# Optimization experiments

Hardware: AMD Instinct MI355X
Metric: run time of the kernel (lower is better)

## Reference

```python
import jax, jax.numpy as jnp
import numpy as np

B, T, L, D, H = 4, 8, 197, 512, 8
DK = D // H
SIM_TH = 0.0
N = T * (L - 1)  # 1568 local tokens

def _ln(x, g, b, eps=1e-5):
    x32 = x.astype(jnp.float32)
    m = jnp.mean(x32, axis=-1, keepdims=True)
    v = jnp.mean((x32 - m) ** 2, axis=-1, keepdims=True)
    return (((x32 - m) * jax.lax.rsqrt(v + eps)) * g + b).astype(x.dtype)

def _qgelu(x):
    return x * jax.nn.sigmoid(1.702 * x)

def _mha(x, w_in, b_in, w_out, b_out):
    # torch nn.MultiheadAttention, x: [S, Bt, D] (seq-first)
    S, Bt, _ = x.shape
    qkv = x @ w_in.T + b_in
    q, k, v = jnp.split(qkv, 3, axis=-1)
    q = q.reshape(S, Bt, H, DK); k = k.reshape(S, Bt, H, DK); v = v.reshape(S, Bt, H, DK)
    scores = jnp.einsum('sbhd,tbhd->bhst', q, k) / jnp.sqrt(jnp.asarray(DK, x.dtype))
    p = jax.nn.softmax(scores, axis=-1)
    o = jnp.einsum('bhst,tbhd->sbhd', p, v).reshape(S, Bt, D)
    return o @ w_out.T + b_out

def _resblock(x, ln1g, ln1b, inw, inb, outw, outb, ln2g, ln2b, fcw, fcb, pw, pb):
    x = x + _mha(_ln(x, ln1g, ln1b), inw, inb, outw, outb)
    h = _qgelu(_ln(x, ln2g, ln2b) @ fcw.T + fcb)
    return x + h @ pw.T + pb

def _build_graph(x, g_mask):
    xd = jax.lax.stop_gradient(x)  # matches x.detach()
    xn = xd / jnp.maximum(jnp.linalg.norm(xd, axis=-1, keepdims=True), 1e-12)
    sim = jnp.einsum('bnd,bmd->bnm', xn, xn)
    adj = jnp.where(sim < SIM_TH, 0.0, sim)
    return adj * g_mask  # t != 1 branch

def _graph_attn(x, mask, wq, bq, wk, bk, wv, bv, wo, bo):
    Bb, Nn, _ = x.shape
    def heads(a):
        return a.reshape(Bb, Nn, H, DK).transpose(0, 2, 1, 3)
    Q = heads(x @ wq.T + bq); K = heads(x @ wk.T + bk); V = heads(x @ wv.T + bv)
    scores = jnp.einsum('bhnd,bhmd->bhnm', Q, K) / jnp.sqrt(jnp.asarray(DK, x.dtype))
    m = mask[:, None]  # [b,1,N,N]
    scores = jnp.where(m == 0, -jnp.inf, scores * m)  # scores*mask then masked_fill(mask==0,-inf)
    p = jax.nn.softmax(scores, axis=-1)
    o = jnp.einsum('bhnm,bhmd->bhnd', p, V).transpose(0, 2, 1, 3).reshape(Bb, Nn, D)
    return o @ wo.T + bo

def _forward(x, proj_w, proj_b,
             m_ln1g, m_ln1b, m_inw, m_inb, m_outw, m_outb,
             m_ln2g, m_ln2b, m_fcw, m_fcb, m_pw, m_pb,
             g_wq, g_bq, g_wk, g_bk, g_wv, g_bv, g_wo, g_bo,
             ln1g, ln1b, a_inw, a_inb, a_outw, a_outb,
             ln2g, ln2b, fcw, fcb, pw, pb, g_mask):
    b, t, l, d = x.shape
    x = x @ proj_w.T + proj_b
    glob = x[:, :, 0, :].transpose(1, 0, 2)  # [t,b,d]
    msg = (m_ln1g, m_ln1b, m_inw, m_inb, m_outw, m_outb, m_ln2g, m_ln2b, m_fcw, m_fcb, m_pw, m_pb)
    glob = _resblock(glob, *msg)
    glob = _resblock(glob, *msg)  # message_attn applied twice (shared weights)
    glob = glob.reshape(1, t, b, d)
    loc = x[:, :, 1:, :].reshape(b, t * (l - 1), d)
    gm = _build_graph(loc, g_mask)
    loc = _graph_attn(loc, gm, g_wq, g_bq, g_wk, g_bk, g_wv, g_bv, g_wo, g_bo)
    loc = loc.reshape(b, t, l - 1, d).transpose(2, 1, 0, 3)  # [l-1,t,b,d]
    y = jnp.concatenate([glob, loc], axis=0).reshape(l, t * b, d)
    y = y + _mha(_ln(y, ln1g, ln1b), a_inw, a_inb, a_outw, a_outb)
    y = y + _qgelu(_ln(y, ln2g, ln2b) @ fcw.T + fcb) @ pw.T + pb
    return y.reshape(l, t, b, d).transpose(2, 1, 0, 3)  # [b,t,l,d]

def setup_inputs() -> dict:
    key = jax.random.key(0)
    ks = jax.random.split(key, 64)
    s = 0.02
    def w(i, shape):
        return jax.random.normal(ks[i], shape, jnp.float32) * s
    ones = jnp.ones((D,), jnp.float32); zeros = jnp.zeros((D,), jnp.float32)
    gm = (jax.random.uniform(ks[60], (N, N)) < 0.5).astype(jnp.float32)
    gm = gm.at[jnp.arange(N), jnp.arange(N)].set(1.0)  # keep self-edges so no row is fully masked
    return dict(
        x=jax.random.normal(ks[0], (B, T, L, D), jnp.float32),
        proj_w=w(1, (D, D)), proj_b=jnp.zeros((D,), jnp.float32),
        m_ln1g=ones, m_ln1b=zeros,
        m_inw=w(2, (3 * D, D)), m_inb=jnp.zeros((3 * D,), jnp.float32),
        m_outw=w(3, (D, D)), m_outb=zeros,
        m_ln2g=ones, m_ln2b=zeros,
        m_fcw=w(4, (4 * D, D)), m_fcb=jnp.zeros((4 * D,), jnp.float32),
        m_pw=w(5, (D, 4 * D)), m_pb=zeros,
        g_wq=w(6, (D, D)), g_bq=zeros, g_wk=w(7, (D, D)), g_bk=zeros,
        g_wv=w(8, (D, D)), g_bv=zeros, g_wo=w(9, (D, D)), g_bo=zeros,
        ln1g=ones, ln1b=zeros,
        a_inw=w(10, (3 * D, D)), a_inb=jnp.zeros((3 * D,), jnp.float32),
        a_outw=w(11, (D, D)), a_outb=zeros,
        ln2g=ones, ln2b=zeros,
        fcw=w(12, (4 * D, D)), fcb=jnp.zeros((4 * D,), jnp.float32),
        pw=w(13, (D, 4 * D)), pb=zeros,
        g_mask=gm,
    )

def reference(x, proj_w, proj_b, m_ln1g, m_ln1b, m_inw, m_inb, m_outw, m_outb,
              m_ln2g, m_ln2b, m_fcw, m_fcb, m_pw, m_pb,
              g_wq, g_bq, g_wk, g_bk, g_wv, g_bv, g_wo, g_bo,
              ln1g, ln1b, a_inw, a_inb, a_outw, a_outb,
              ln2g, ln2b, fcw, fcb, pw, pb, g_mask):
    return _forward(x, proj_w, proj_b, m_ln1g, m_ln1b, m_inw, m_inb, m_outw, m_outb,
                    m_ln2g, m_ln2b, m_fcw, m_fcb, m_pw, m_pb,
                    g_wq, g_bq, g_wk, g_bk, g_wv, g_bv, g_wo, g_bo,
                    ln1g, ln1b, a_inw, a_inb, a_outw, a_outb,
                    ln2g, ln2b, fcw, fcb, pw, pb, g_mask)
```

## Files before the change

### kernel.cpp

```cpp
#include <hip/hip_runtime.h>
#include <hip/hip_bf16.h>

typedef unsigned short u16;
typedef __attribute__((ext_vector_type(8))) short bf16x8;
typedef __attribute__((ext_vector_type(4))) float f32x4;

#define FINF __builtin_huge_valf()

static __device__ __forceinline__ float bf2f(u16 v){ union{unsigned u; float f;} c; c.u = ((unsigned)v)<<16; return c.f; }
static __device__ __forceinline__ u16 f2bf(float f){ union{__hip_bfloat16 h; u16 u;} c; c.h = __float2bfloat16(f); return c.u; }
static __device__ __forceinline__ bf16x8 scale8(bf16x8 v, float s){
  bf16x8 o;
  #pragma unroll
  for (int e=0;e<8;e++) o[e] = (short)f2bf(bf2f((u16)v[e])*s);
  return o;
}

static __device__ __forceinline__ void gload16(const void* g, void* l){
  __builtin_amdgcn_global_load_lds(
      (const __attribute__((address_space(1))) void*)g,
      (__attribute__((address_space(3))) void*)l, 16, 0, 0);
}

#define WAIT_VM0()   { asm volatile("s_waitcnt vmcnt(0)" ::: "memory"); __builtin_amdgcn_sched_barrier(0); }
#define BARRIER()    { __builtin_amdgcn_sched_barrier(0); __builtin_amdgcn_s_barrier(); __builtin_amdgcn_sched_barrier(0); }

struct CvtArgs {
  const float* src[14];
  u16* dst[14];
  int n[14];
};
__global__ __launch_bounds__(256) void cvt_multi(CvtArgs a){
  int seg = blockIdx.y;
  const float* s = a.src[seg]; u16* d = a.dst[seg]; int n = a.n[seg];
  for (int i = (blockIdx.x*256 + threadIdx.x)*4; i < n; i += gridDim.x*256*4){
    float4 v = *(const float4*)(s + i);
    ushort4 o = { f2bf(v.x), f2bf(v.y), f2bf(v.z), f2bf(v.w) };
    *(ushort4*)(d + i) = o;
  }
}

__global__ __launch_bounds__(256) void concat_bias(const float* a, const float* b, const float* c, float* o){
  int i = blockIdx.x*256 + threadIdx.x;
  o[i] = i < 512 ? a[i] : (i < 1024 ? b[i-512] : c[i-1024]);
}

template<int BM, int EPI, int MW>
__global__ __launch_bounds__(256,MW) void gemm_nt(
    const u16* __restrict__ A, const u16* __restrict__ Bw,
    const float* __restrict__ bias, const float* aux, void* out,
    int M, int Nn, int K, int ldc, long aBatch, long bBatch, long cBatch)
{
  constexpr int MI = BM/32;
  constexpr int WSPAN = BM/2;
  __shared__ __align__(16) u16 a_lds[2*BM*64];
  __shared__ __align__(16) u16 b_lds[2*128*64];
  const int z = blockIdx.z;
  const u16* Az = A + (long)z*aBatch;
  const u16* Bz = Bw + (long)z*bBatch;
  const int n0 = blockIdx.x*128, m0 = blockIdx.y*BM;
  const int t = threadIdx.x, lane = t & 63, wave = t >> 6;
  const int wr = wave >> 1, wc = wave & 1;
  const int r = lane & 15, kq = lane >> 4;

  const int srow = t >> 3;
  const int scol = ((t&7)*8) ^ ((srow&7)<<3);
  int rowA[MI], rowB[4];
  #pragma unroll
  for (int i=0;i<MI;i++){ int ga = m0 + i*32 + srow; rowA[i] = ga < M ? ga : M-1; }
  #pragma unroll
  for (int i=0;i<4;i++){ int gb = n0 + i*32 + srow; rowB[i] = gb < Nn ? gb : Nn-1; }

  f32x4 acc[MI][4] = {};
  const int nkt = K >> 6;

  auto STAGE = [&](int kt, int buf){
    const long koff = (long)kt*64 + scol;
    #pragma unroll
    for (int i=0;i<MI;i++)
      gload16(Az + (long)rowA[i]*K + koff, (char*)a_lds + buf*(BM*128) + i*4096 + wave*1024);
    #pragma unroll
    for (int i=0;i<4;i++)
      gload16(Bz + (long)rowB[i]*K + koff, (char*)b_lds + buf*16384 + i*4096 + wave*1024);
  };

  STAGE(0,0);
  WAIT_VM0(); BARRIER();
  for (int kt=0; kt<nkt; kt++){
    const int cur = kt&1;
    if (kt+1 < nkt) STAGE(kt+1, cur^1);
    const u16* al = a_lds + cur*BM*64;
    const u16* bl = b_lds + cur*8192;
    #pragma unroll
    for (int kk=0; kk<2; kk++){
      bf16x8 af[MI], bfr[4];
      #pragma unroll
      for (int i=0;i<MI;i++){
        int rw = wr*WSPAN + i*16 + r;
        af[i] = *(const bf16x8*)&al[rw*64 + ((kk*32 + kq*8) ^ ((rw&7)<<3))];
      }
      #pragma unroll
      for (int j=0;j<4;j++){
        int rw = wc*64 + j*16 + r;
        bfr[j] = *(const bf16x8*)&bl[rw*64 + ((kk*32 + kq*8) ^ ((rw&7)<<3))];
      }
      #pragma unroll
      for (int i=0;i<MI;i++)
        #pragma unroll
        for (int j=0;j<4;j++)
          acc[i][j] = __builtin_amdgcn_mfma_f32_16x16x32_bf16(af[i], bfr[j], acc[i][j], 0,0,0);
    }
    WAIT_VM0(); BARRIER();
  }

  #pragma unroll
  for (int i=0;i<MI;i++){
    #pragma unroll
    for (int j=0;j<4;j++){
      int gcol = n0 + wc*64 + j*16 + r;
      if (gcol >= Nn) continue;
      float bv = bias ? bias[gcol] : 0.f;
      #pragma unroll
      for (int rr=0; rr<4; rr++){
        int grow = m0 + wr*WSPAN + i*16 + kq*4 + rr;
        if (grow >= M) continue;
        float v = acc[i][j][rr] + bv;
        if constexpr (EPI==0){
          ((float*)out)[(long)z*cBatch + (long)grow*ldc + gcol] = v;
        } else if constexpr (EPI==1){
          ((u16*)out)[(long)z*cBatch + (long)grow*ldc + gcol] = f2bf(v);
        } else if constexpr (EPI==2){
          long idx = (long)z*cBatch + (long)grow*ldc + gcol;
          ((float*)out)[idx] = aux[idx] + v;
        } else if constexpr (EPI==3){
          float g = v / (1.f + __expf(-1.702f*v));
          ((u16*)out)[(long)z*cBatch + (long)grow*ldc + gcol] = f2bf(g);
        } else if constexpr (EPI==4){
          float adj = v < 0.f ? 0.f : v;
          float gmv = aux[(long)grow*Nn + gcol];
          ((u16*)out)[(long)z*cBatch + (long)grow*ldc + gcol] = f2bf(adj*gmv);
        } else if constexpr (EPI==5){
          int b = grow/1568, n = grow%1568, tt = n/196, lp = n%196;
          int yrow = (1+lp)*32 + tt*4 + b;
          ((float*)out)[(long)yrow*ldc + gcol] = v;
        } else if constexpr (EPI==6){
          long idx = (long)grow*ldc + gcol;
          int l = grow>>5, rb = grow&31, tt = rb>>2, bb = rb&3;
          ((float*)out)[((long)((bb*8+tt)*197) + l)*512 + gcol] = aux[idx] + v;
        }
      }
    }
  }
}

__global__ __launch_bounds__(256) void transpose_v(
    const u16* __restrict__ src, u16* __restrict__ vt,
    int nrows, long zofs, long nofs, int vcol0, int outld)
{
  __shared__ u16 tile[64][66];
  const int t = threadIdx.x;
  const int nt = blockIdx.x, h = blockIdx.y, z = blockIdx.z;
  const int n0 = nt*64;
  const int rlo = t>>3, c0 = (t&7)*8;
  #pragma unroll
  for (int i=0;i<2;i++){
    int nl = i*32 + rlo;
    int n = n0 + nl; int nc = n < nrows ? n : nrows-1;
    const u16* s = src + (long)z*zofs + (long)nc*nofs + vcol0 + h*64 + c0;
    uint4 v = *(const uint4*)s;
    bool dead = n >= nrows;
    #pragma unroll
    for (int e=0;e<8;e++) tile[nl][c0+e] = dead ? (u16)0 : ((const u16*)&v)[e];
  }
  __syncthreads();
  #pragma unroll
  for (int i=0;i<2;i++){
    int d = i*32 + rlo;
    u16 tmp[8];
    #pragma unroll
    for (int e=0;e<8;e++) tmp[e] = tile[c0+e][d];
    int ncol = n0 + c0;
    if (ncol + 8 <= outld){
      u16* dst = vt + ((long)((z*8+h)*64 + d))*outld + ncol;
      *(uint4*)dst = *(uint4*)tmp;
    }
  }
}

template<bool MASKED>
__global__ __launch_bounds__(256, MASKED?2:3) void flash2(
    const u16* __restrict__ QKV, const u16* __restrict__ VT,
    const u16* __restrict__ gmask, u16* __restrict__ Out,
    int nq, int nk, int nqb, long qBatch, long qRow,
    long oBatch, long oRow, long gmBatch, int vtld)
{
  __shared__ __align__(16) u16 k_lds[2*4096];
  __shared__ __align__(16) u16 v_lds[2*4096];
  __shared__ __align__(16) u16 g_lds[MASKED ? 2*4096 : 8];
  __shared__ __align__(16) u16 p_lds[4][16*72];
  int h, z, qb;
  if constexpr (MASKED){
    int id = blockIdx.x;
    int a = id>>6, c = id&7; h = (id>>3)&7;
    int G = a*8 + c;
    if (G >= 4*nqb) return;
    z = G / nqb; qb = G % nqb;
  } else {
    qb = blockIdx.x; h = blockIdx.y; z = blockIdx.z;
  }
  const int t = threadIdx.x, lane = t&63, wave = t>>6;
  const int r = lane&15, kq = lane>>4;
  const u16* Qb = QKV + (long)z*qBatch + h*64;
  const u16* Kb = Qb + 512;
  const u16* Vt = VT + (long)(z*8+h)*64*vtld;
  const u16* Gz = MASKED ? (gmask + (long)z*gmBatch) : nullptr;
  const int qt0 = qb*64;
  const int q0  = qt0 + wave*16;

  bf16x8 qf0, qf1;
  { int qi = q0 + r; if (qi > nq-1) qi = nq-1;
    const u16* qp = Qb + (long)qi*qRow + kq*8;
    qf0 = scale8(*(const bf16x8*)qp, 0.125f);
    qf1 = scale8(*(const bf16x8*)(qp+32), 0.125f); }

  const int srow = t>>3;
  const int scol = ((t&7)*8) ^ ((srow&7)<<3);

  auto stage = [&](int kt, int buf){
    #pragma unroll
    for (int i=0;i<2;i++){
      int j = kt*64 + i*32 + srow; if (j > nk-1) j = nk-1;
      gload16(Kb + (long)j*qRow + scol, (char*)k_lds + buf*8192 + i*4096 + wave*1024);
    }
    #pragma unroll
    for (int i=0;i<2;i++){
      int d = i*32 + srow;
      gload16(Vt + (long)d*vtld + kt*64 + scol, (char*)v_lds + buf*8192 + i*4096 + wave*1024);
    }
    if constexpr (MASKED){
      #pragma unroll
      for (int i=0;i<2;i++){
        int qr = qt0 + i*32 + srow; if (qr > nq-1) qr = nq-1;
        gload16(Gz + (long)qr*nk + kt*64 + scol, (char*)g_lds + buf*8192 + i*4096 + wave*1024);
      }
    }
  };

  bf16x8 ONES;
  #pragma unroll
  for (int e=0;e<8;e++) ONES[e] = (short)0x3F80;

  float m_[4] = {-FINF,-FINF,-FINF,-FINF};
  f32x4 o_[4] = {}; f32x4 ol = {};

  const int nkt = (nk + 63) >> 6;
  stage(0,0);
  __syncthreads();
  for (int kt=0; kt<nkt; kt++){
    const int cur = kt&1;
    if (kt+1 < nkt) stage(kt+1, cur^1);

    float s[4][4];
    const u16* kl = k_lds + cur*4096;
    #pragma unroll
    for (int sub=0; sub<4; sub++){
      int rw = sub*16 + r; int sw = (rw&7)<<3;
      bf16x8 kf0 = *(const bf16x8*)&kl[rw*64 + ((kq*8) ^ sw)];
      bf16x8 kf1 = *(const bf16x8*)&kl[rw*64 + ((32 + kq*8) ^ sw)];
      f32x4 sc = {};
      sc = __builtin_amdgcn_mfma_f32_16x16x32_bf16(qf0, kf0, sc, 0,0,0);
      sc = __builtin_amdgcn_mfma_f32_16x16x32_bf16(qf1, kf1, sc, 0,0,0);
      #pragma unroll
      for (int rr=0;rr<4;rr++) s[sub][rr] = sc[rr];
    }
    #pragma unroll
    for (int sub=0; sub<4; sub++){
      int key = kt*64 + sub*16 + r;
      bool kdead = key >= nk;
      #pragma unroll
      for (int rr=0;rr<4;rr++){
        float sv = s[sub][rr];
        if constexpr (MASKED){
          int lrow = wave*16 + kq*4 + rr;
          u16 g = g_lds[cur*4096 + lrow*64 + ((sub*16+r) ^ ((lrow&7)<<3))];
          if (g == 0 || kdead) sv = -FINF; else sv *= bf2f(g);
        } else {
          if (kdead) sv = -FINF;
        }
        s[sub][rr] = sv;
      }
    }
    #pragma unroll
    for (int rr=0;rr<4;rr++){
      float mx = fmaxf(fmaxf(s[0][rr],s[1][rr]), fmaxf(s[2][rr],s[3][rr]));
      #pragma unroll
      for (int d=1; d<16; d<<=1) mx = fmaxf(mx, __shfl_xor(mx, d));
      float mnew = fmaxf(m_[rr], mx);
      float fac = (m_[rr] == -FINF) ? 0.f : __expf(m_[rr] - mnew);
      #pragma unroll
      for (int sub=0;sub<4;sub++)
        s[sub][rr] = (s[sub][rr] == -FINF) ? 0.f : __expf(s[sub][rr] - mnew);
      m_[rr] = mnew;
      o_[0][rr]*=fac; o_[1][rr]*=fac; o_[2][rr]*=fac; o_[3][rr]*=fac; ol[rr]*=fac;
    }
    #pragma unroll
    for (int rr=0;rr<4;rr++){
      int prow = kq*4+rr;
      #pragma unroll
      for (int sub=0;sub<4;sub++)
        p_lds[wave][prow*72 + ((sub*16+r) ^ ((prow&7)<<3))] = f2bf(s[sub][rr]);
    }
    const u16* vl = v_lds + cur*4096;
    #pragma unroll
    for (int c=0;c<2;c++){
      bf16x8 pf = *(const bf16x8*)&p_lds[wave][r*72 + ((c*32 + kq*8) ^ ((r&7)<<3))];
      #pragma unroll
      for (int j=0;j<4;j++){
        int rw = j*16 + r;
        bf16x8 vf = *(const bf16x8*)&vl[rw*64 + ((c*32 + kq*8) ^ ((rw&7)<<3))];
        o_[j] = __builtin_amdgcn_mfma_f32_16x16x32_bf16(pf, vf, o_[j], 0,0,0);
      }
      ol = __builtin_amdgcn_mfma_f32_16x16x32_bf16(pf, ONES, ol, 0,0,0);
    }
    __syncthreads();
  }

  #pragma unroll
  for (int rr=0;rr<4;rr++){
    int qrow = q0 + kq*4 + rr;
    if (qrow >= nq) continue;
    float inv = ol[rr] > 0.f ? 1.f/ol[rr] : 0.f;
    #pragma unroll
    for (int j=0;j<4;j++)
      Out[(long)z*oBatch + (long)qrow*oRow + h*64 + j*16 + r] = f2bf(o_[j][rr]*inv);
  }
}

__global__ __launch_bounds__(256) void ln_rows(const float* __restrict__ in,
    const float* __restrict__ g, const float* __restrict__ b, u16* __restrict__ out, int rows)
{
  int wave = threadIdx.x >> 6, lane = threadIdx.x & 63;
  int row = blockIdx.x*4 + wave;
  if (row >= rows) return;
  const float4* x = (const float4*)(in + (long)row*512);
  float4 v0 = x[lane], v1 = x[lane+64];
  float s  = v0.x+v0.y+v0.z+v0.w + v1.x+v1.y+v1.z+v1.w;
  float ss = v0.x*v0.x+v0.y*v0.y+v0.z*v0.z+v0.w*v0.w + v1.x*v1.x+v1.y*v1.y+v1.z*v1.z+v1.w*v1.w;
  #pragma unroll
  for (int d=1; d<64; d<<=1){ s += __shfl_xor(s,d); ss += __shfl_xor(ss,d); }
  float mean = s * (1.f/512.f);
  float var = ss * (1.f/512.f) - mean*mean;
  float rs = rsqrtf(var + 1e-5f);
  const float4* gg = (const float4*)g; const float4* bb = (const float4*)b;
  float4 g0 = gg[lane], g1 = gg[lane+64], b0 = bb[lane], b1 = bb[lane+64];
  u16* o = out + (long)row*512;
  ushort4 o0 = { f2bf((v0.x-mean)*rs*g0.x + b0.x), f2bf((v0.y-mean)*rs*g0.y + b0.y),
                 f2bf((v0.z-mean)*rs*g0.z + b0.z), f2bf((v0.w-mean)*rs*g0.w + b0.w) };
  ushort4 o1 = { f2bf((v1.x-mean)*rs*g1.x + b1.x), f2bf((v1.y-mean)*rs*g1.y + b1.y),
                 f2bf((v1.z-mean)*rs*g1.z + b1.z), f2bf((v1.w-mean)*rs*g1.w + b1.w) };
  *(ushort4*)(o + lane*4) = o0;
  *(ushort4*)(o + 256 + lane*4) = o1;
}

__global__ __launch_bounds__(256) void locprep(const float* __restrict__ y0,
    u16* __restrict__ xn, u16* __restrict__ locb)
{
  int wave = threadIdx.x >> 6, lane = threadIdx.x & 63;
  int rr = blockIdx.x*4 + wave;
  int bb = rr/1568, n = rr%1568, tt = n/196, lp = n%196;
  const float4* x = (const float4*)(y0 + ((long)((bb*8+tt)*197) + 1 + lp)*512);
  float4 v0 = x[lane], v1 = x[lane+64];
  float ss = v0.x*v0.x+v0.y*v0.y+v0.z*v0.z+v0.w*v0.w + v1.x*v1.x+v1.y*v1.y+v1.z*v1.z+v1.w*v1.w;
  #pragma unroll
  for (int d=1; d<64; d<<=1) ss += __shfl_xor(ss,d);
  float sc = 1.f / fmaxf(sqrtf(ss), 1e-12f);
  u16* ox = xn + (long)rr*512;
  u16* ol = locb + (long)rr*512;
  ushort4 a0 = { f2bf(v0.x*sc), f2bf(v0.y*sc), f2bf(v0.z*sc), f2bf(v0.w*sc) };
  ushort4 a1 = { f2bf(v1.x*sc), f2bf(v1.y*sc), f2bf(v1.z*sc), f2bf(v1.w*sc) };
  ushort4 c0 = { f2bf(v0.x), f2bf(v0.y), f2bf(v0.z), f2bf(v0.w) };
  ushort4 c1 = { f2bf(v1.x), f2bf(v1.y), f2bf(v1.z), f2bf(v1.w) };
  *(ushort4*)(ox + lane*4) = a0;  *(ushort4*)(ox + 256 + lane*4) = a1;
  *(ushort4*)(ol + lane*4) = c0;  *(ushort4*)(ol + 256 + lane*4) = c1;
}

__global__ __launch_bounds__(64) void msg_attn(const u16* __restrict__ mqkv, u16* __restrict__ matt){
  __shared__ float q_s[8][64], k_s[8][64], v_s[8][64];
  int bh = blockIdx.x; int bt = bh>>3, h = bh&7;
  int lane = threadIdx.x;
  int row = lane>>3, cc = (lane&7)*8;
  #pragma unroll
  for (int e=0;e<8;e++){
    long base = (long)(row*4 + bt)*1536 + h*64 + cc + e;
    q_s[row][cc+e] = bf2f(mqkv[base]);
    k_s[row][cc+e] = bf2f(mqkv[base + 512]);
    v_s[row][cc+e] = bf2f(mqkv[base + 1024]);
  }
  __syncthreads();
  int q = lane>>3, k = lane&7;
  float s = 0.f;
  #pragma unroll 16
  for (int d=0; d<64; d++) s += q_s[q][d]*k_s[k][d];
  s *= 0.125f;
  float mx = s;
  #pragma unroll
  for (int d=1; d<8; d<<=1) mx = fmaxf(mx, __shfl_xor(mx,d));
  float p = __expf(s - mx), ps = p;
  #pragma unroll
  for (int d=1; d<8; d<<=1) ps += __shfl_xor(ps,d);
  p /= ps;
  for (int d=0; d<64; d++){
    float ov = p * v_s[k][d];
    #pragma unroll
    for (int m=1; m<8; m<<=1) ov += __shfl_xor(ov,m);
    if (k == (d>>3)) matt[(long)(q*4 + bt)*512 + h*64 + d] = f2bf(ov);
  }
}

__global__ __launch_bounds__(256) void gather_glob(const float* __restrict__ y0, float* __restrict__ glob){
  int idx = blockIdx.x*256 + threadIdx.x;
  int orow = idx>>9, d = idx&511;
  int tt = orow>>2, bb = orow&3;
  glob[idx] = y0[((long)(bb*8+tt)*197)*512 + d];
}
__global__ __launch_bounds__(256) void copy32(const float* __restrict__ glob, float* __restrict__ y){
  int idx = blockIdx.x*256 + threadIdx.x;
  y[idx] = glob[idx];
}

extern "C" void kernel_launch(void* const* d_in, const int* in_sizes, int n_in,
                              void* d_out, int out_size, void* d_ws, size_t ws_size,
                              hipStream_t stream)
{
  const float* x      = (const float*)d_in[0];
  const float* proj_w = (const float*)d_in[1];
  const float* proj_b = (const float*)d_in[2];
  const float* m_ln1g = (const float*)d_in[3];
  const float* m_ln1b = (const float*)d_in[4];
  const float* m_inw  = (const float*)d_in[5];
  const float* m_inb  = (const float*)d_in[6];
  const float* m_outw = (const float*)d_in[7];
  const float* m_outb = (const float*)d_in[8];
  const float* m_ln2g = (const float*)d_in[9];
  const float* m_ln2b = (const float*)d_in[10];
  const float* m_fcw  = (const float*)d_in[11];
  const float* m_fcb  = (const float*)d_in[12];
  const float* m_pw   = (const float*)d_in[13];
  const float* m_pb   = (const float*)d_in[14];
  const float* g_wq = (const float*)d_in[15]; const float* g_bq = (const float*)d_in[16];
  const float* g_wk = (const float*)d_in[17]; const float* g_bk = (const float*)d_in[18];
  const float* g_wv = (const float*)d_in[19]; const float* g_bv = (const float*)d_in[20];
  const float* g_wo = (const float*)d_in[21]; const float* g_bo = (const float*)d_in[22];
  const float* ln1g = (const float*)d_in[23]; const float* ln1b = (const float*)d_in[24];
  const float* a_inw = (const float*)d_in[25]; const float* a_inb = (const float*)d_in[26];
  const float* a_outw = (const float*)d_in[27]; const float* a_outb = (const float*)d_in[28];
  const float* ln2g = (const float*)d_in[29]; const float* ln2b = (const float*)d_in[30];
  const float* fcw = (const float*)d_in[31]; const float* fcb = (const float*)d_in[32];
  const float* pw = (const float*)d_in[33]; const float* pb = (const float*)d_in[34];
  const float* g_mask = (const float*)d_in[35];

  if (ws_size < (size_t)99753984) return;

  char* ws = (char*)d_ws;
  u16* WB = (u16*)ws;
  const long WPROJ=0, WMIN=262144, WMOUT=1048576, WMFC=1310720, WMP=2359296,
             WGQ=3407872, WGK=3670016, WGV=3932160, WGO=4194304,
             WAIN=4456448, WAOUT=5242880, WFC=5505024, WP=6553600;
  float* y0   = (float*)(ws + 15204352);
  float* y    = (float*)(ws + 28114944);
  u16* lnbuf  = (u16*)(ws + 41025536);
  u16* vtg    = (u16*)(ws + 41025536);
  u16* locb   = (u16*)(ws + 47480832);
  u16* qkv    = (u16*)(ws + 53903360);
  u16* xb     = (u16*)(ws + 73269248);
  u16* gm     = (u16*)(ws + 73269248);
  u16* vt2    = (u16*)(ws + 73269248);
  u16* hbuf   = (u16*)(ws + 73269248);
  u16* obuf   = (u16*)(ws + 92938240);
  float* glob = (float*)(ws + 99393536);
  u16* mlnb   = (u16*)(ws + 99459072);
  u16* mqkv   = (u16*)(ws + 99491840);
  u16* matt   = (u16*)(ws + 99590144);
  u16* mh     = (u16*)(ws + 99622912);
  float* gbias = (float*)(ws + 99622912);

  CvtArgs ca;
  auto setseg=[&](int i, const float* s, u16* d, int n){ ca.src[i]=s; ca.dst[i]=d; ca.n[i]=n; };
  setseg(0,  x,      xb,       6304*512);
  setseg(1,  proj_w, WB+WPROJ, 262144);
  setseg(2,  m_inw,  WB+WMIN,  786432);
  setseg(3,  m_outw, WB+WMOUT, 262144);
  setseg(4,  m_fcw,  WB+WMFC,  1048576);
  setseg(5,  m_pw,   WB+WMP,   1048576);
  setseg(6,  g_wq,   WB+WGQ,   262144);
  setseg(7,  g_wk,   WB+WGK,   262144);
  setseg(8,  g_wv,   WB+WGV,   262144);
  setseg(9,  g_wo,   WB+WGO,   262144);
  setseg(10, a_inw,  WB+WAIN,  786432);
  setseg(11, a_outw, WB+WAOUT, 262144);
  setseg(12, fcw,    WB+WFC,   1048576);
  setseg(13, pw,     WB+WP,    1048576);
  cvt_multi<<<dim3(128,14), 256, 0, stream>>>(ca);

  gemm_nt<64,0,3><<<dim3(4,99), 256, 0, stream>>>(xb, WB+WPROJ, proj_b, nullptr, y0, 6304,512,512,512, 0,0,0);

  gather_glob<<<64,256,0,stream>>>(y0, glob);

  for (int it=0; it<2; ++it){
    ln_rows<<<8,256,0,stream>>>(glob, m_ln1g, m_ln1b, mlnb, 32);
    gemm_nt<64,1,3><<<dim3(12,1),256,0,stream>>>(mlnb, WB+WMIN, m_inb, nullptr, mqkv, 32,1536,512,1536, 0,0,0);
    msg_attn<<<32,64,0,stream>>>(mqkv, matt);
    gemm_nt<64,2,3><<<dim3(4,1),256,0,stream>>>(matt, WB+WMOUT, m_outb, glob, glob, 32,512,512,512, 0,0,0);
    ln_rows<<<8,256,0,stream>>>(glob, m_ln2g, m_ln2b, mlnb, 32);
    gemm_nt<64,3,3><<<dim3(16,1),256,0,stream>>>(mlnb, WB+WMFC, m_fcb, nullptr, mh, 32,2048,512,2048, 0,0,0);
    gemm_nt<64,2,3><<<dim3(4,1),256,0,stream>>>(mh, WB+WMP, m_pb, glob, glob, 32,512,2048,512, 0,0,0);
  }

  concat_bias<<<6,256,0,stream>>>(g_bq, g_bk, g_bv, gbias);

  locprep<<<1568,256,0,stream>>>(y0, lnbuf, locb);

  gemm_nt<128,4,2><<<dim3(13,13,4),256,0,stream>>>(lnbuf, lnbuf, nullptr, g_mask, gm,
      1568,1568,512,1568, 1568L*512, 1568L*512, 1568L*1568);

  gemm_nt<128,1,2><<<dim3(12,49),256,0,stream>>>(locb, WB+WGQ, gbias, nullptr, qkv, 6272,1536,512,1536, 0,0,0);

  transpose_v<<<dim3(25,8,4),256,0,stream>>>(qkv, vtg, 1568, 1568L*1536, 1536L, 1024, 1568);

  flash2<true><<<832,256,0,stream>>>(qkv, vtg, gm, obuf,
      1568,1568,25, 1568L*1536, 1536, 1568L*512, 512, 1568L*1568, 1568);

  gemm_nt<64,5,3><<<dim3(4,98),256,0,stream>>>(obuf, WB+WGO, g_bo, nullptr, y, 6272,512,512,512, 0,0,0);

  copy32<<<64,256,0,stream>>>(glob, y);

  ln_rows<<<1576,256,0,stream>>>(y, ln1g, ln1b, lnbuf, 6304);
  gemm_nt<128,1,2><<<dim3(12,50),256,0,stream>>>(lnbuf, WB+WAIN, a_inb, nullptr, qkv, 6304,1536,512,1536, 0,0,0);
  transpose_v<<<dim3(4,8,32),256,0,stream>>>(qkv, vt2, 197, 1536L, 32L*1536, 1024, 256);
  flash2<false><<<dim3(4,8,32),256,0,stream>>>(qkv, vt2, nullptr, obuf,
      197,197,4, 1536, 32L*1536, 512, 32L*512, 0, 256);
  gemm_nt<64,2,3><<<dim3(4,99),256,0,stream>>>(obuf, WB+WAOUT, a_outb, y, y, 6304,512,512,512, 0,0,0);

  ln_rows<<<1576,256,0,stream>>>(y, ln2g, ln2b, lnbuf, 6304);
  gemm_nt<128,3,2><<<dim3(16,50),256,0,stream>>>(lnbuf, WB+WFC, fcb, nullptr, hbuf, 6304,2048,512,2048, 0,0,0);
  gemm_nt<64,6,3><<<dim3(4,99),256,0,stream>>>(hbuf, WB+WP, pb, y, (float*)d_out, 6304,512,2048,512, 0,0,0);
}
```

Before: 608.0 us.

## Transpose flash attention to key-major scores, load V and mask directly into registers

The attention kernel now computes S^T by swapping the MFMA operands. Each lane then holds one query row, so the row max needs only two cross-lane shuffles instead of a 16-lane butterfly. V fragments and graph-mask values are loaded from global memory straight into registers instead of being staged through LDS, which cuts LDS to the K double buffer plus a P tile and raises the occupancy target to 4 blocks. Several large GEMMs also switch from 128-row tiles to 64-row tiles with more blocks, trading data reuse for higher occupancy. The unstaged global loads of V and the mask may add latency, since they are no longer overlapped by the async LDS pipeline.

```diff
diff --git a/kernel.cpp b/kernel.cpp
--- a/kernel.cpp
+++ b/kernel.cpp
@@ -188,16 +188,14 @@
 }
 
 template<bool MASKED>
-__global__ __launch_bounds__(256, MASKED?2:3) void flash2(
+__global__ __launch_bounds__(256,4) void flash3(
     const u16* __restrict__ QKV, const u16* __restrict__ VT,
     const u16* __restrict__ gmask, u16* __restrict__ Out,
     int nq, int nk, int nqb, long qBatch, long qRow,
     long oBatch, long oRow, long gmBatch, int vtld)
 {
   __shared__ __align__(16) u16 k_lds[2*4096];
-  __shared__ __align__(16) u16 v_lds[2*4096];
-  __shared__ __align__(16) u16 g_lds[MASKED ? 2*4096 : 8];
-  __shared__ __align__(16) u16 p_lds[4][16*72];
+  __shared__ __align__(16) u16 p_lds[4][1024];
   int h, z, qb;
   if constexpr (MASKED){
     int id = blockIdx.x;
@@ -213,126 +211,129 @@
   const u16* Qb = QKV + (long)z*qBatch + h*64;
   const u16* Kb = Qb + 512;
   const u16* Vt = VT + (long)(z*8+h)*64*vtld;
-  const u16* Gz = MASKED ? (gmask + (long)z*gmBatch) : nullptr;
   const int qt0 = qb*64;
   const int q0  = qt0 + wave*16;
+  const int q   = q0 + r;
+  const int qc  = q < nq ? q : nq-1;
+  const u16* Gq = MASKED ? (gmask + (long)z*gmBatch + (long)qc*nk) : nullptr;
 
   bf16x8 qf0, qf1;
-  { int qi = q0 + r; if (qi > nq-1) qi = nq-1;
-    const u16* qp = Qb + (long)qi*qRow + kq*8;
+  { const u16* qp = Qb + (long)qc*qRow + kq*8;
     qf0 = scale8(*(const bf16x8*)qp, 0.125f);
     qf1 = scale8(*(const bf16x8*)(qp+32), 0.125f); }
 
   const int srow = t>>3;
   const int scol = ((t&7)*8) ^ ((srow&7)<<3);
 
-  auto stage = [&](int kt, int buf){
+  auto stage_k = [&](int kt, int buf){
     #pragma unroll
     for (int i=0;i<2;i++){
       int j = kt*64 + i*32 + srow; if (j > nk-1) j = nk-1;
       gload16(Kb + (long)j*qRow + scol, (char*)k_lds + buf*8192 + i*4096 + wave*1024);
     }
-    #pragma unroll
-    for (int i=0;i<2;i++){
-      int d = i*32 + srow;
-      gload16(Vt + (long)d*vtld + kt*64 + scol, (char*)v_lds + buf*8192 + i*4096 + wave*1024);
-    }
-    if constexpr (MASKED){
-      #pragma unroll
-      for (int i=0;i<2;i++){
-        int qr = qt0 + i*32 + srow; if (qr > nq-1) qr = nq-1;
-        gload16(Gz + (long)qr*nk + kt*64 + scol, (char*)g_lds + buf*8192 + i*4096 + wave*1024);
-      }
-    }
   };
 
   bf16x8 ONES;
   #pragma unroll
   for (int e=0;e<8;e++) ONES[e] = (short)0x3F80;
 
-  float m_[4] = {-FINF,-FINF,-FINF,-FINF};
-  f32x4 o_[4] = {}; f32x4 ol = {};
+  float m_ = -FINF;
+  f32x4 o_[4] = {};  f32x4 l_ = {};
 
   const int nkt = (nk + 63) >> 6;
-  stage(0,0);
+  stage_k(0,0);
   __syncthreads();
   for (int kt=0; kt<nkt; kt++){
     const int cur = kt&1;
-    if (kt+1 < nkt) stage(kt+1, cur^1);
-
-    float s[4][4];
+    if (kt+1 < nkt) stage_k(kt+1, cur^1);
+
+    uint4 vfr[2][4];
+    #pragma unroll
+    for (int c=0;c<2;c++)
+      #pragma unroll
+      for (int j=0;j<4;j++)
+        vfr[c][j] = *(const uint4*)(Vt + (long)(j*16+r)*vtld + kt*64 + c*32 + kq*8);
+    ushort4 gv[4];
+    if constexpr (MASKED){
+      #pragma unroll
+      for (int sub=0;sub<4;sub++)
+        gv[sub] = *(const ushort4*)(Gq + kt*64 + sub*16 + kq*4);
+    }
+
     const u16* kl = k_lds + cur*4096;
+    float p[4][4];
     #pragma unroll
     for (int sub=0; sub<4; sub++){
       int rw = sub*16 + r; int sw = (rw&7)<<3;
       bf16x8 kf0 = *(const bf16x8*)&kl[rw*64 + ((kq*8) ^ sw)];
       bf16x8 kf1 = *(const bf16x8*)&kl[rw*64 + ((32 + kq*8) ^ sw)];
       f32x4 sc = {};
-      sc = __builtin_amdgcn_mfma_f32_16x16x32_bf16(qf0, kf0, sc, 0,0,0);
-      sc = __builtin_amdgcn_mfma_f32_16x16x32_bf16(qf1, kf1, sc, 0,0,0);
-      #pragma unroll
-      for (int rr=0;rr<4;rr++) s[sub][rr] = sc[rr];
-    }
-    #pragma unroll
-    for (int sub=0; sub<4; sub++){
-      int key = kt*64 + sub*16 + r;
-      bool kdead = key >= nk;
+      sc = __builtin_amdgcn_mfma_f32_16x16x32_bf16(kf0, qf0, sc, 0,0,0);
+      sc = __builtin_amdgcn_mfma_f32_16x16x32_bf16(kf1, qf1, sc, 0,0,0);
       #pragma unroll
       for (int rr=0;rr<4;rr++){
-        float sv = s[sub][rr];
+        float sv = sc[rr];
+        int key = kt*64 + sub*16 + kq*4 + rr;
         if constexpr (MASKED){
-          int lrow = wave*16 + kq*4 + rr;
-          u16 g = g_lds[cur*4096 + lrow*64 + ((sub*16+r) ^ ((lrow&7)<<3))];
-          if (g == 0 || kdead) sv = -FINF; else sv *= bf2f(g);
+          u16 g = ((const u16*)&gv[sub])[rr];
+          sv = (g == 0 || key >= nk) ? -FINF : sv * bf2f(g);
         } else {
-          if (kdead) sv = -FINF;
+          if (key >= nk) sv = -FINF;
         }
-        s[sub][rr] = sv;
+        p[sub][rr] = sv;
       }
     }
-    #pragma unroll
-    for (int rr=0;rr<4;rr++){
-      float mx = fmaxf(fmaxf(s[0][rr],s[1][rr]), fmaxf(s[2][rr],s[3][rr]));
-      #pragma unroll
-      for (int d=1; d<16; d<<=1) mx = fmaxf(mx, __shfl_xor(mx, d));
-      float mnew = fmaxf(m_[rr], mx);
-      float fac = (m_[rr] == -FINF) ? 0.f : __expf(m_[rr] - mnew);
-      #pragma unroll
-      for (int sub=0;sub<4;sub++)
-        s[sub][rr] = (s[sub][rr] == -FINF) ? 0.f : __expf(s[sub][rr] - mnew);
-      m_[rr] = mnew;
-      o_[0][rr]*=fac; o_[1][rr]*=fac; o_[2][rr]*=fac; o_[3][rr]*=fac; ol[rr]*=fac;
-    }
-    #pragma unroll
-    for (int rr=0;rr<4;rr++){
-      int prow = kq*4+rr;
-      #pragma unroll
-      for (int sub=0;sub<4;sub++)
-        p_lds[wave][prow*72 + ((sub*16+r) ^ ((prow&7)<<3))] = f2bf(s[sub][rr]);
-    }
-    const u16* vl = v_lds + cur*4096;
+
+    float mx;
+    { float a0 = fmaxf(fmaxf(p[0][0],p[0][1]), fmaxf(p[0][2],p[0][3]));
+      float a1 = fmaxf(fmaxf(p[1][0],p[1][1]), fmaxf(p[1][2],p[1][3]));
+      float a2 = fmaxf(fmaxf(p[2][0],p[2][1]), fmaxf(p[2][2],p[2][3]));
+      float a3 = fmaxf(fmaxf(p[3][0],p[3][1]), fmaxf(p[3][2],p[3][3]));
+      mx = fmaxf(fmaxf(a0,a1), fmaxf(a2,a3)); }
+    mx = fmaxf(mx, __shfl_xor(mx, 16));
+    mx = fmaxf(mx, __shfl_xor(mx, 32));
+    float mnew = fmaxf(m_, mx);
+    float fac = (m_ == -FINF) ? 0.f : __expf(m_ - mnew);
+    #pragma unroll
+    for (int j=0;j<4;j++){ o_[j][0]*=fac; o_[j][1]*=fac; o_[j][2]*=fac; o_[j][3]*=fac; }
+    l_[0]*=fac; l_[1]*=fac; l_[2]*=fac; l_[3]*=fac;
+    m_ = mnew;
+
+    #pragma unroll
+    for (int sub=0;sub<4;sub++){
+      float e0 = (p[sub][0] == -FINF) ? 0.f : __expf(p[sub][0] - mnew);
+      float e1 = (p[sub][1] == -FINF) ? 0.f : __expf(p[sub][1] - mnew);
+      float e2 = (p[sub][2] == -FINF) ? 0.f : __expf(p[sub][2] - mnew);
+      float e3 = (p[sub][3] == -FINF) ? 0.f : __expf(p[sub][3] - mnew);
+      unsigned u0, u1;
+      asm volatile("v_cvt_pk_bf16_f32 %0, %1, %2" : "=v"(u0) : "v"(e0), "v"(e1));
+      asm volatile("v_cvt_pk_bf16_f32 %0, %1, %2" : "=v"(u1) : "v"(e2), "v"(e3));
+      uint2 w; w.x = u0; w.y = u1;
+      int idx = r*64 + ((sub*16 + kq*4) ^ ((r&7)<<3));
+      *(uint2*)&p_lds[wave][idx] = w;
+    }
+
     #pragma unroll
     for (int c=0;c<2;c++){
-      bf16x8 pf = *(const bf16x8*)&p_lds[wave][r*72 + ((c*32 + kq*8) ^ ((r&7)<<3))];
+      bf16x8 pf = *(const bf16x8*)&p_lds[wave][r*64 + ((c*32 + kq*8) ^ ((r&7)<<3))];
       #pragma unroll
       for (int j=0;j<4;j++){
-        int rw = j*16 + r;
-        bf16x8 vf = *(const bf16x8*)&vl[rw*64 + ((c*32 + kq*8) ^ ((rw&7)<<3))];
-        o_[j] = __builtin_amdgcn_mfma_f32_16x16x32_bf16(pf, vf, o_[j], 0,0,0);
+        bf16x8 vf = *(const bf16x8*)&vfr[c][j];
+        o_[j] = __builtin_amdgcn_mfma_f32_16x16x32_bf16(vf, pf, o_[j], 0,0,0);
       }
-      ol = __builtin_amdgcn_mfma_f32_16x16x32_bf16(pf, ONES, ol, 0,0,0);
+      l_ = __builtin_amdgcn_mfma_f32_16x16x32_bf16(ONES, pf, l_, 0,0,0);
     }
     __syncthreads();
   }
 
-  #pragma unroll
-  for (int rr=0;rr<4;rr++){
-    int qrow = q0 + kq*4 + rr;
-    if (qrow >= nq) continue;
-    float inv = ol[rr] > 0.f ? 1.f/ol[rr] : 0.f;
-    #pragma unroll
-    for (int j=0;j<4;j++)
-      Out[(long)z*oBatch + (long)qrow*oRow + h*64 + j*16 + r] = f2bf(o_[j][rr]*inv);
+  float inv = l_[0] > 0.f ? 1.f/l_[0] : 0.f;
+  if (q < nq){
+    #pragma unroll
+    for (int j=0;j<4;j++){
+      ushort4 ov = { f2bf(o_[j][0]*inv), f2bf(o_[j][1]*inv),
+                     f2bf(o_[j][2]*inv), f2bf(o_[j][3]*inv) };
+      *(ushort4*)(Out + (long)z*oBatch + (long)q*oRow + h*64 + j*16 + kq*4) = ov;
+    }
   }
 }
 
@@ -520,14 +521,14 @@
 
   locprep<<<1568,256,0,stream>>>(y0, lnbuf, locb);
 
-  gemm_nt<128,4,2><<<dim3(13,13,4),256,0,stream>>>(lnbuf, lnbuf, nullptr, g_mask, gm,
+  gemm_nt<64,4,3><<<dim3(13,25,4),256,0,stream>>>(lnbuf, lnbuf, nullptr, g_mask, gm,
       1568,1568,512,1568, 1568L*512, 1568L*512, 1568L*1568);
 
-  gemm_nt<128,1,2><<<dim3(12,49),256,0,stream>>>(locb, WB+WGQ, gbias, nullptr, qkv, 6272,1536,512,1536, 0,0,0);
+  gemm_nt<64,1,3><<<dim3(12,98),256,0,stream>>>(locb, WB+WGQ, gbias, nullptr, qkv, 6272,1536,512,1536, 0,0,0);
 
   transpose_v<<<dim3(25,8,4),256,0,stream>>>(qkv, vtg, 1568, 1568L*1536, 1536L, 1024, 1568);
 
-  flash2<true><<<832,256,0,stream>>>(qkv, vtg, gm, obuf,
+  flash3<true><<<832,256,0,stream>>>(qkv, vtg, gm, obuf,
       1568,1568,25, 1568L*1536, 1536, 1568L*512, 512, 1568L*1568, 1568);
 
   gemm_nt<64,5,3><<<dim3(4,98),256,0,stream>>>(obuf, WB+WGO, g_bo, nullptr, y, 6272,512,512,512, 0,0,0);
@@ -535,13 +536,13 @@
   copy32<<<64,256,0,stream>>>(glob, y);
 
   ln_rows<<<1576,256,0,stream>>>(y, ln1g, ln1b, lnbuf, 6304);
-  gemm_nt<128,1,2><<<dim3(12,50),256,0,stream>>>(lnbuf, WB+WAIN, a_inb, nullptr, qkv, 6304,1536,512,1536, 0,0,0);
+  gemm_nt<64,1,3><<<dim3(12,99),256,0,stream>>>(lnbuf, WB+WAIN, a_inb, nullptr, qkv, 6304,1536,512,1536, 0,0,0);
   transpose_v<<<dim3(4,8,32),256,0,stream>>>(qkv, vt2, 197, 1536L, 32L*1536, 1024, 256);
-  flash2<false><<<dim3(4,8,32),256,0,stream>>>(qkv, vt2, nullptr, obuf,
+  flash3<false><<<dim3(4,8,32),256,0,stream>>>(qkv, vt2, nullptr, obuf,
       197,197,4, 1536, 32L*1536, 512, 32L*512, 0, 256);
   gemm_nt<64,2,3><<<dim3(4,99),256,0,stream>>>(obuf, WB+WAOUT, a_outb, y, y, 6304,512,512,512, 0,0,0);
 
   ln_rows<<<1576,256,0,stream>>>(y, ln2g, ln2b, lnbuf, 6304);
-  gemm_nt<128,3,2><<<dim3(16,50),256,0,stream>>>(lnbuf, WB+WFC, fcb, nullptr, hbuf, 6304,2048,512,2048, 0,0,0);
+  gemm_nt<64,3,3><<<dim3(16,99),256,0,stream>>>(lnbuf, WB+WFC, fcb, nullptr, hbuf, 6304,2048,512,2048, 0,0,0);
   gemm_nt<64,6,3><<<dim3(4,99),256,0,stream>>>(hbuf, WB+WP, pb, y, (float*)d_out, 6304,512,2048,512, 0,0,0);
 }
```

New measurement: 569.5 us. -6.3%, faster.
